# Optimization experiments

Hardware: AMD Instinct MI355X
Metric: run time of the kernel (lower is better)

## Reference

```python
import jax, jax.numpy as jnp
import numpy as np

N_LAYERS = 4
N, D = 50000, 80          # nodes, hidden (hardcoded 80 in Net)
E, ED = 800000, 16        # edges, edge_attr dim
PE_DIM = 37               # pe_embedding=37
G = 256                   # number of graphs in the batch
MSG = 2 * D + ED          # per-edge message dim: cat([x_i, x_j, edge_attr]) = 176
AGG = 4 * MSG             # mean/min/max/std -> 704
SCL = 3 * AGG             # identity/amplification/attenuation -> 2112
EPS_BN = 1e-5

# `deg` init kwarg: degree histogram; PNAConvSimple uses avg log-degree for scalers
_DEG_HIST = np.array([0, 5000, 10000, 15000, 10000, 5000, 3000, 2000], dtype=np.float64)
_ds = np.arange(len(_DEG_HIST), dtype=np.float64)
AVG_LOG_DEG = float((np.log(_ds + 1.0) * _DEG_HIST).sum() / _DEG_HIST.sum())


def setup_inputs() -> dict:
    key = jax.random.key(0)
    ks = jax.random.split(key, 20)
    sd = 0.05
    inp = {
        "x": jax.random.normal(ks[0], (N, D), jnp.float32),
        "edge_index": jax.random.randint(ks[1], (2, E), 0, N, jnp.int32),
        "edge_attr": jax.random.normal(ks[2], (E, ED), jnp.float32),
        "PE": jax.random.normal(ks[3], (N, PE_DIM), jnp.float32),
        "snorm": jnp.ones((N, 1), jnp.float32),
        "batch": jnp.sort(jax.random.randint(ks[4], (N,), 0, G, jnp.int32)),
        # per-layer params (stacked over 4 layers)
        "pe_w": jax.random.normal(ks[5], (N_LAYERS, PE_DIM, D), jnp.float32) * sd,
        "pe_b": jnp.zeros((N_LAYERS, D), jnp.float32),
        "conv_w": jax.random.normal(ks[6], (N_LAYERS, SCL, D), jnp.float32) * sd,
        "conv_b": jnp.zeros((N_LAYERS, D), jnp.float32),
        "bn_g": jnp.ones((N_LAYERS, D), jnp.float32),
        "bn_b": jnp.zeros((N_LAYERS, D), jnp.float32),
        # MLP head 80 -> 40 -> 20 -> 1
        "w1": jax.random.normal(ks[7], (D, 40), jnp.float32) * sd,
        "b1": jnp.zeros((40,), jnp.float32),
        "w2": jax.random.normal(ks[8], (40, 20), jnp.float32) * sd,
        "b2": jnp.zeros((20,), jnp.float32),
        "w3": jax.random.normal(ks[9], (20, 1), jnp.float32) * sd,
        "b3": jnp.zeros((1,), jnp.float32),
    }
    return inp


def _pna_layer(x, src, tgt, edge_attr, pe, pe_w, pe_b, W, b, g, beta):
    # node features enriched with PE embedding (pe_embedding=37 -> 80)
    xp = x + pe @ pe_w + pe_b                                  # [N, D]
    h = jnp.concatenate([xp[tgt], xp[src], edge_attr], axis=-1)  # [E, MSG]
    one = jnp.ones((h.shape[0],), h.dtype)
    cnt = jax.ops.segment_sum(one, tgt, N)
    d = jnp.maximum(cnt, 1.0)[:, None]                         # in-degree, clamped >= 1
    s = jax.ops.segment_sum(h, tgt, N)
    mean = s / d
    sq = jax.ops.segment_sum(h * h, tgt, N) / d
    std = jnp.sqrt(jax.nn.relu(sq - mean * mean) + 1e-5)
    mx = jax.ops.segment_max(h, tgt, N)
    mx = jnp.where(jnp.isfinite(mx), mx, 0.0)
    mn = jax.ops.segment_min(h, tgt, N)
    mn = jnp.where(jnp.isfinite(mn), mn, 0.0)
    agg = jnp.concatenate([mean, mn, mx, std], axis=-1)        # [N, AGG]
    logd = jnp.log(d + 1.0)
    out = jnp.concatenate(
        [agg, agg * (logd / AVG_LOG_DEG), agg * (AVG_LOG_DEG / logd)], axis=-1
    )                                                          # [N, SCL]
    out = out @ W + b                                          # post_nn Linear -> [N, D]
    # BatchNorm over nodes (batch statistics; deterministic)
    mu = out.mean(0)
    var = out.var(0)
    out = (out - mu) * jax.lax.rsqrt(var + EPS_BN) * g + beta
    return jax.nn.relu(out) + x                                # residual (dropout off in eval)


def reference(x, edge_index, edge_attr, PE, snorm, batch,
              pe_w, pe_b, conv_w, conv_b, bn_g, bn_b,
              w1, b1, w2, b2, w3, b3):
    src, tgt = edge_index[0], edge_index[1]
    for l in range(N_LAYERS):
        x = _pna_layer(x, src, tgt, edge_attr, PE,
                       pe_w[l], pe_b[l], conv_w[l], conv_b[l], bn_g[l], bn_b[l])
    # global_mean_pool over graphs
    gcnt = jnp.maximum(jax.ops.segment_sum(jnp.ones((N,), x.dtype), batch, G), 1.0)[:, None]
    pooled = jax.ops.segment_sum(x, batch, G) / gcnt           # [G, D]
    h = jax.nn.relu(pooled @ w1 + b1)
    h = jax.nn.relu(h @ w2 + b2)
    return h @ w3 + b3                                         # [G, 1]
```

## Files before the change

### kernel.cpp

```cpp
#include <hip/hip_runtime.h>
#include <stdint.h>

#define NN 50000
#define DD 80
#define NE 800000
#define EDIM 16
#define PED 37
#define NG 256
#define NLAY 4
#define KZ 480
#define NOUT 240
#define MPAD 50048
#define NBLK (MPAD/128)
#define NB 196
#define KP 64
#define NPE (NLAY*DD)
#define AVG_LD 1.4059212841460147f
#define S5 0.0031622776601683794f

typedef __bf16 bf16x8 __attribute__((ext_vector_type(8)));
typedef float f32x4 __attribute__((ext_vector_type(4)));

__device__ __forceinline__ unsigned short f2bf(float f){
  union { float f; unsigned u; } v; v.f = f;
  return (unsigned short)((v.u + 0x7fffu + ((v.u >> 16) & 1u)) >> 16);
}
__device__ __forceinline__ float bf2f(unsigned short u){
  union { unsigned u; float f; } v; v.u = ((unsigned)u) << 16; return v.f;
}
__device__ __forceinline__ unsigned packbf(float a, float b){
  return (unsigned)f2bf(a) | ((unsigned)f2bf(b) << 16);
}

#define R_HIST NE
#define R_ZP8  (((MPAD-NN)*KZ)/8)
#define R_WP   (NLAY*NOUT*KZ)
#define R_PEB  (MPAD*KP)
#define R_PWT  (NPE*KP)
#define R_TOT  (R_HIST + R_ZP8 + R_WP + R_PEB + R_PWT)

__global__ void k_init(const int* __restrict__ ei, int* deg, unsigned short* Z,
                       const float* __restrict__ conv_w, unsigned short* __restrict__ WcT,
                       const float* __restrict__ PE,
                       const float* __restrict__ pe_w, const float* __restrict__ pe_b,
                       unsigned short* __restrict__ PEb, unsigned short* __restrict__ pwT){
  int idx = blockIdx.x*blockDim.x + threadIdx.x;
  if(idx < R_HIST){ atomicAdd(&deg[ei[NE + idx]], 1); return; }
  int r1 = idx - R_HIST;
  if(r1 < R_ZP8){
    uint4* zp = (uint4*)(Z + (size_t)NN*KZ);
    zp[r1] = (uint4){0,0,0,0};
    return;
  }
  int r2 = r1 - R_ZP8;
  if(r2 < R_WP){
    int l = r2 / (NOUT*KZ);
    int k = r2 % (NOUT*KZ);
    int j = k / KZ;
    int r = k % KZ;
    int ks = j / DD, c = j % DD;
    const float* cw = conv_w + (size_t)l*2112*DD;
    float val = 0.0f;
    if(r < 384){
      int stat = r/96, m = r%96;
      val = cw[(size_t)(ks*704 + stat*176 + 80 + m)*DD + c];
    } else if(r < 464){
      int m = r - 384;
      int b = ks*704 + m;
      val = cw[(size_t)b*DD + c] + cw[(size_t)(b+176)*DD + c] + cw[(size_t)(b+352)*DD + c];
    } else if(r == 464){
      float s = 0.0f; int b = ks*704 + 528;
      for(int m=0;m<80;++m) s += cw[(size_t)(b+m)*DD + c];
      val = S5 * s;
    }
    WcT[(size_t)l*NOUT*KZ + k] = f2bf(val);
    return;
  }
  int r3 = r2 - R_WP;
  if(r3 < R_PEB){
    int i = r3 / KP, k = r3 % KP;
    float v = 0.0f;
    if(i < NN){
      if(k < PED) v = PE[(size_t)i*PED + k];
      else if(k == PED) v = 1.0f;
    }
    PEb[r3] = f2bf(v);
    return;
  }
  int r4 = r3 - R_PEB;
  if(r4 < R_PWT){
    int j = r4 / KP, k = r4 % KP;
    int l = j / DD, c = j % DD;
    float v = 0.0f;
    if(k < PED) v = pe_w[(size_t)(l*PED + k)*DD + c];
    else if(k == PED) v = pe_b[l*DD + c];
    pwT[r4] = f2bf(v);
  }
}

__global__ __launch_bounds__(256) void k_pegemm(
    const unsigned short* __restrict__ PEb, const unsigned short* __restrict__ pwT,
    const float* __restrict__ x0, unsigned short* __restrict__ pe_all,
    unsigned short* __restrict__ xpb){
  int tid = threadIdx.x;
  int wave = tid >> 6, lane = tid & 63;
  int r = lane & 15, q = lane >> 4;
  int m0 = blockIdx.x*64 + wave*16;
  const unsigned short* Ap = PEb + (size_t)(m0 + r)*KP + q*8;
  const unsigned short* Bp = pwT + (size_t)r*KP + q*8;
  f32x4 acc[20];
  #pragma unroll
  for(int i=0;i<20;++i) acc[i] = (f32x4){0.f,0.f,0.f,0.f};
  #pragma unroll
  for(int k0=0; k0<KP; k0+=32){
    bf16x8 a = *(const bf16x8*)(Ap + k0);
    #pragma unroll
    for(int ct=0; ct<20; ++ct){
      bf16x8 b = *(const bf16x8*)(Bp + (size_t)ct*16*KP + k0);
      acc[ct] = __builtin_amdgcn_mfma_f32_16x16x32_bf16(a, b, acc[ct], 0, 0, 0);
    }
  }
  #pragma unroll
  for(int rr=0; rr<4; ++rr){
    int grow = m0 + q*4 + rr;
    #pragma unroll
    for(int ct=0; ct<20; ++ct){
      int c = ct*16 + r;
      float v = acc[ct][rr];
      pe_all[(size_t)grow*NPE + c] = f2bf(v);
      if(c < DD && grow < NN)
        xpb[(size_t)grow*DD + c] = f2bf(x0[(size_t)grow*DD + c] + v);
    }
  }
}

__global__ void k_scan1(const int* __restrict__ deg, int* bsum){
  __shared__ int red[256];
  int i = blockIdx.x*256 + threadIdx.x;
  int v = (i < NN) ? deg[i] : 0;
  red[threadIdx.x] = v; __syncthreads();
  for(int d=128; d>0; d>>=1){
    if(threadIdx.x < d) red[threadIdx.x] += red[threadIdx.x + d];
    __syncthreads();
  }
  if(threadIdx.x == 0) bsum[blockIdx.x] = red[0];
}

__global__ void k_scan2(const int* __restrict__ bsum, int* bbase, int* off){
  __shared__ int s[256];
  int t = threadIdx.x;
  int v = (t < NB) ? bsum[t] : 0;
  s[t] = v; __syncthreads();
  for(int d=1; d<256; d<<=1){
    int u = (t >= d) ? s[t-d] : 0;
    __syncthreads();
    s[t] += u;
    __syncthreads();
  }
  if(t < NB) bbase[t] = s[t] - v;
  if(t == NB-1) off[NN] = s[t];
}

__global__ void k_scan3(const int* __restrict__ deg, const int* __restrict__ bbase,
                        int* off, int* pos){
  __shared__ int s[256];
  int t = threadIdx.x;
  int i = blockIdx.x*256 + t;
  int v = (i < NN) ? deg[i] : 0;
  s[t] = v; __syncthreads();
  for(int d=1; d<256; d<<=1){
    int u = (t >= d) ? s[t-d] : 0;
    __syncthreads();
    s[t] += u;
    __syncthreads();
  }
  int excl = s[t] - v + bbase[blockIdx.x];
  if(i < NN){ off[i] = excl; pos[i] = excl; }
}

__global__ void k_fill(const int* __restrict__ ei, const float* __restrict__ ea,
                       int* pos, int* esrc, unsigned short* __restrict__ ea_b){
  int e = blockIdx.x*blockDim.x + threadIdx.x;
  if(e >= NE) return;
  int t = ei[NE + e];
  int idx = atomicAdd(&pos[t], 1);
  esrc[idx] = ei[e];
  const float4* s = (const float4*)(ea + (size_t)e*EDIM);
  float4 f0=s[0], f1=s[1], f2=s[2], f3=s[3];
  unsigned short tmp[16];
  tmp[0]=f2bf(f0.x); tmp[1]=f2bf(f0.y); tmp[2]=f2bf(f0.z); tmp[3]=f2bf(f0.w);
  tmp[4]=f2bf(f1.x); tmp[5]=f2bf(f1.y); tmp[6]=f2bf(f1.z); tmp[7]=f2bf(f1.w);
  tmp[8]=f2bf(f2.x); tmp[9]=f2bf(f2.y); tmp[10]=f2bf(f2.z); tmp[11]=f2bf(f2.w);
  tmp[12]=f2bf(f3.x); tmp[13]=f2bf(f3.y); tmp[14]=f2bf(f3.z); tmp[15]=f2bf(f3.w);
  uint4* d = (uint4*)(ea_b + (size_t)idx*EDIM);
  d[0] = *(uint4*)&tmp[0];
  d[1] = *(uint4*)&tmp[8];
}

__global__ __launch_bounds__(256) void k_agg(
    const unsigned short* __restrict__ xpb, const unsigned short* __restrict__ ea_b,
    const int* __restrict__ esrc, const int* __restrict__ off,
    unsigned short* __restrict__ Z, float2* __restrict__ sc){
  int g = blockIdx.x*4 + (threadIdx.x >> 6);
  if(g >= NN) return;
  int lane = threadIdx.x & 63;
  int h = lane >> 5, t = lane & 31;
  int lo = off[g], hi = off[g+1];
  int d = hi - lo;
  float s0=0,s1=0,s2=0,q0=0,q1=0,q2=0;
  const float INF = __builtin_huge_valf();
  float mn0=INF,mn1=INF,mn2=INF,mx0=-INF,mx1=-INF,mx2=-INF;

  auto edge = [&](int j){
    int sr = esrc[j];
    const unsigned* xr32 = (const unsigned*)(xpb + (size_t)sr*DD);
    unsigned w = xr32[t];
    union {unsigned u; float f;} ua, ub;
    ua.u = w << 16; ub.u = w & 0xffff0000u;
    float v0 = ua.f, v1 = ub.f;
    unsigned short u2 = (t < 16) ? xpb[(size_t)sr*DD + 64 + t]
                                 : ea_b[(size_t)j*EDIM + (t - 16)];
    float v2 = bf2f(u2);
    s0+=v0; q0+=v0*v0; mn0=fminf(mn0,v0); mx0=fmaxf(mx0,v0);
    s1+=v1; q1+=v1*v1; mn1=fminf(mn1,v1); mx1=fmaxf(mx1,v1);
    s2+=v2; q2+=v2*v2; mn2=fminf(mn2,v2); mx2=fmaxf(mx2,v2);
  };
  int j = lo + h;
  for(; j + 2 < hi; j += 4){ edge(j); edge(j+2); }
  if(j < hi) edge(j);

  s0 += __shfl_xor(s0,32,64); s1 += __shfl_xor(s1,32,64); s2 += __shfl_xor(s2,32,64);
  q0 += __shfl_xor(q0,32,64); q1 += __shfl_xor(q1,32,64); q2 += __shfl_xor(q2,32,64);
  mn0 = fminf(mn0, __shfl_xor(mn0,32,64));
  mn1 = fminf(mn1, __shfl_xor(mn1,32,64));
  mn2 = fminf(mn2, __shfl_xor(mn2,32,64));
  mx0 = fmaxf(mx0, __shfl_xor(mx0,32,64));
  mx1 = fmaxf(mx1, __shfl_xor(mx1,32,64));
  mx2 = fmaxf(mx2, __shfl_xor(mx2,32,64));

  float dc = (float)(d>0?d:1);
  float inv = 1.0f/dc;
  float m0=s0*inv, m1=s1*inv, m2=s2*inv;
  float sd0 = sqrtf(fmaxf(q0*inv - m0*m0, 0.0f) + 1e-5f);
  float sd1 = sqrtf(fmaxf(q1*inv - m1*m1, 0.0f) + 1e-5f);
  float sd2 = sqrtf(fmaxf(q2*inv - m2*m2, 0.0f) + 1e-5f);
  if(d==0){ mn0=mn1=mn2=0.0f; mx0=mx1=mx2=0.0f; }

  unsigned* zr32 = (unsigned*)(Z + (size_t)g*KZ);
  unsigned short* zr = (unsigned short*)zr32;
  if(h == 0){
    zr32[t]       = packbf(m0, m1);
    zr32[48 + t]  = packbf(mn0, mn1);
    zr32[96 + t]  = packbf(mx0, mx1);
    zr32[144 + t] = packbf(sd0, sd1);
    zr[64 + t]        = f2bf(m2);
    zr[96 + 64 + t]   = f2bf(mn2);
    zr[192 + 64 + t]  = f2bf(mx2);
    zr[288 + 64 + t]  = f2bf(sd2);
  } else {
    const unsigned* xg32 = (const unsigned*)(xpb + (size_t)g*DD);
    zr32[192 + t] = (d>0) ? xg32[t] : 0u;
    if(t < 8)  zr32[224 + t] = (d>0) ? xg32[32 + t] : 0u;
    if(t >= 8 && t < 16) zr32[232 + (t-8)] = (t==8) ? 0x3F80u : 0u;
  }
  if(lane == 0){
    float logd = logf(dc + 1.0f);
    sc[g] = make_float2(logd/AVG_LD, AVG_LD/logd);
  }
}

__global__ __launch_bounds__(256) void k_gemm(
    const unsigned short* __restrict__ Z, const unsigned short* __restrict__ WcT,
    const float2* __restrict__ sc, const float* __restrict__ bias,
    float* __restrict__ outb, float* __restrict__ partial){
  __shared__ float sred[4][160];
  int tid = threadIdx.x;
  int wave = tid >> 6, lane = tid & 63;
  int r = lane & 15, q = lane >> 4;
  int m0 = blockIdx.x*128 + wave*32;
  const unsigned short* Ap = Z + (size_t)(m0 + r)*KZ + q*8;
  const unsigned short* Bp = WcT + (size_t)r*KZ + q*8;
  f32x4 acc0[15], acc1[15];
  #pragma unroll
  for(int i=0;i<15;++i){ acc0[i]=(f32x4){0.f,0.f,0.f,0.f}; acc1[i]=(f32x4){0.f,0.f,0.f,0.f}; }
  #pragma unroll 1
  for(int k0=0; k0<KZ; k0+=32){
    bf16x8 a0 = *(const bf16x8*)(Ap + k0);
    bf16x8 a1 = *(const bf16x8*)(Ap + 16*KZ + k0);
    #pragma unroll
    for(int ct=0; ct<15; ++ct){
      bf16x8 b = *(const bf16x8*)(Bp + (size_t)ct*16*KZ + k0);
      acc0[ct] = __builtin_amdgcn_mfma_f32_16x16x32_bf16(a0, b, acc0[ct], 0, 0, 0);
      acc1[ct] = __builtin_amdgcn_mfma_f32_16x16x32_bf16(a1, b, acc1[ct], 0, 0, 0);
    }
  }
  float colS[5], colQ[5];
  #pragma unroll
  for(int ct=0; ct<5; ++ct){ colS[ct]=0.f; colQ[ct]=0.f; }
  #pragma unroll
  for(int rr=0; rr<4; ++rr){
    int grow = m0 + q*4 + rr;
    if(grow < NN){
      float2 ab = sc[grow];
      #pragma unroll
      for(int ct=0; ct<5; ++ct){
        int c = ct*16 + r;
        float v = acc0[ct][rr] + ab.x*acc0[ct+5][rr] + ab.y*acc0[ct+10][rr] + bias[c];
        outb[(size_t)grow*DD + c] = v;
        colS[ct] += v; colQ[ct] += v*v;
      }
    }
  }
  #pragma unroll
  for(int rr=0; rr<4; ++rr){
    int grow = m0 + 16 + q*4 + rr;
    if(grow < NN){
      float2 ab = sc[grow];
      #pragma unroll
      for(int ct=0; ct<5; ++ct){
        int c = ct*16 + r;
        float v = acc1[ct][rr] + ab.x*acc1[ct+5][rr] + ab.y*acc1[ct+10][rr] + bias[c];
        outb[(size_t)grow*DD + c] = v;
        colS[ct] += v; colQ[ct] += v*v;
      }
    }
  }
  #pragma unroll
  for(int ct=0; ct<5; ++ct){
    colS[ct] += __shfl_xor(colS[ct], 16, 64);
    colS[ct] += __shfl_xor(colS[ct], 32, 64);
    colQ[ct] += __shfl_xor(colQ[ct], 16, 64);
    colQ[ct] += __shfl_xor(colQ[ct], 32, 64);
  }
  if(q == 0){
    #pragma unroll
    for(int ct=0; ct<5; ++ct){
      int c = ct*16 + r;
      sred[wave][c] = colS[ct];
      sred[wave][80+c] = colQ[ct];
    }
  }
  __syncthreads();
  if(tid < 160){
    partial[(size_t)blockIdx.x*160 + tid] =
      sred[0][tid] + sred[1][tid] + sred[2][tid] + sred[3][tid];
  }
}

__global__ void k_bnfin(const float* __restrict__ partial, float* __restrict__ murs){
  __shared__ float red[1024];
  __shared__ float tot[160];
  int tid = threadIdx.x;
  int c = tid % 160, stripe = tid / 160;
  float s = 0.0f;
  if(tid < 960){
    for(int b=stripe; b<NBLK; b+=6) s += partial[(size_t)b*160 + c];
  }
  red[tid] = s; __syncthreads();
  if(tid < 160){
    float t2 = 0.0f;
    for(int k=0;k<6;++k) t2 += red[k*160 + tid];
    tot[tid] = t2;
  }
  __syncthreads();
  if(tid < 80){
    float mu = tot[tid] / (float)NN;
    float var = tot[80+tid] / (float)NN - mu*mu;
    murs[tid] = mu;
    murs[80+tid] = rsqrtf(var + 1e-5f);
  }
}

__global__ __launch_bounds__(256) void k_apply(
    const float* __restrict__ outb, const float* __restrict__ murs,
    const float* __restrict__ g_, const float* __restrict__ b_,
    const float* __restrict__ xc, float* __restrict__ xn,
    const unsigned short* __restrict__ pe_all, unsigned short* __restrict__ xpb,
    int lnext, int do_xp){
  int idx = blockIdx.x*blockDim.x + threadIdx.x;
  if(idx >= NN*20) return;
  int c = (idx % 20) * 4;
  float4 o = ((const float4*)outb)[idx];
  float4 x = ((const float4*)xc)[idx];
  float4 r;
  r.x = fmaxf((o.x - murs[c+0])*murs[80+c+0]*g_[c+0] + b_[c+0], 0.0f) + x.x;
  r.y = fmaxf((o.y - murs[c+1])*murs[80+c+1]*g_[c+1] + b_[c+1], 0.0f) + x.y;
  r.z = fmaxf((o.z - murs[c+2])*murs[80+c+2]*g_[c+2] + b_[c+2], 0.0f) + x.z;
  r.w = fmaxf((o.w - murs[c+3])*murs[80+c+3]*g_[c+3] + b_[c+3], 0.0f) + x.w;
  ((float4*)xn)[idx] = r;
  if(do_xp){
    int i = idx / 20;
    uint2 pe = ((const uint2*)pe_all)[(size_t)i*(NPE/4) + lnext*(DD/4) + (idx % 20)];
    float p0 = bf2f((unsigned short)(pe.x & 0xffffu));
    float p1 = bf2f((unsigned short)(pe.x >> 16));
    float p2 = bf2f((unsigned short)(pe.y & 0xffffu));
    float p3 = bf2f((unsigned short)(pe.y >> 16));
    uint2 out;
    out.x = packbf(r.x + p0, r.y + p1);
    out.y = packbf(r.z + p2, r.w + p3);
    ((uint2*)xpb)[idx] = out;
  }
}

__device__ __forceinline__ int lbound(const int* b, int n, int v){
  int lo=0, hi=n;
  while(lo < hi){ int mid = (lo+hi)>>1; if(b[mid] < v) lo = mid+1; else hi = mid; }
  return lo;
}

__global__ __launch_bounds__(640) void k_poolmlp(
    const float* __restrict__ xf, const int* __restrict__ batch,
    const float* __restrict__ w1, const float* __restrict__ b1,
    const float* __restrict__ w2, const float* __restrict__ b2,
    const float* __restrict__ w3, const float* __restrict__ b3,
    float* __restrict__ out){
  __shared__ float red[8][80];
  __shared__ float pooled[80];
  __shared__ float h1[40], h2[20];
  int g = blockIdx.x;
  int tid = threadIdx.x;
  int stripe = tid / 80, c = tid % 80;
  int lo = lbound(batch, NN, g), hi = lbound(batch, NN, g+1);
  float s = 0.0f;
  for(int i = lo + stripe; i < hi; i += 8) s += xf[(size_t)i*DD + c];
  red[stripe][c] = s;
  __syncthreads();
  if(tid < 80){
    float tsum = 0.0f;
    #pragma unroll
    for(int k=0;k<8;++k) tsum += red[k][tid];
    int cnt = hi - lo;
    pooled[tid] = tsum / (float)(cnt > 0 ? cnt : 1);
  }
  __syncthreads();
  if(tid < 40){
    float h = b1[tid];
    for(int cc=0; cc<80; ++cc) h += pooled[cc] * w1[cc*40 + tid];
    h1[tid] = fmaxf(h, 0.0f);
  }
  __syncthreads();
  if(tid < 20){
    float h = b2[tid];
    for(int cc=0; cc<40; ++cc) h += h1[cc] * w2[cc*20 + tid];
    h2[tid] = fmaxf(h, 0.0f);
  }
  __syncthreads();
  if(tid == 0){
    float o = b3[0];
    for(int j=0;j<20;++j) o += h2[j] * w3[j];
    out[g] = o;
  }
}

extern "C" void kernel_launch(void* const* d_in, const int* in_sizes, int n_in,
                              void* d_out, int out_size, void* d_ws, size_t ws_size,
                              hipStream_t stream){
  const float* x0     = (const float*)d_in[0];
  const int*   ei     = (const int*)d_in[1];
  const float* ea     = (const float*)d_in[2];
  const float* PE     = (const float*)d_in[3];
  const int*   batch  = (const int*)d_in[5];
  const float* pe_w   = (const float*)d_in[6];
  const float* pe_b   = (const float*)d_in[7];
  const float* conv_w = (const float*)d_in[8];
  const float* conv_b = (const float*)d_in[9];
  const float* bn_g   = (const float*)d_in[10];
  const float* bn_b   = (const float*)d_in[11];
  const float* w1 = (const float*)d_in[12];
  const float* b1 = (const float*)d_in[13];
  const float* w2 = (const float*)d_in[14];
  const float* b2 = (const float*)d_in[15];
  const float* w3 = (const float*)d_in[16];
  const float* b3 = (const float*)d_in[17];
  float* dout = (float*)d_out;

  char* p = (char*)d_ws;
  auto alloc = [&](size_t bytes)->char*{
    char* r = p; p += (bytes + 255) & ~(size_t)255; return r;
  };
  int* deg  = (int*)alloc((size_t)NN*4);
  int* pos  = (int*)alloc((size_t)NN*4);
  int* off  = (int*)alloc((size_t)(NN+1)*4);
  int* bsum = (int*)alloc((size_t)NB*4);
  int* bbase= (int*)alloc((size_t)NB*4);
  int* esrc = (int*)alloc((size_t)NE*4);
  unsigned short* ea_b = (unsigned short*)alloc((size_t)NE*EDIM*2);
  unsigned short* xpb  = (unsigned short*)alloc((size_t)NN*DD*2);
  unsigned short* PEb  = (unsigned short*)alloc((size_t)MPAD*KP*2);
  unsigned short* pwT  = (unsigned short*)alloc((size_t)NPE*KP*2);
  unsigned short* pe_all = (unsigned short*)alloc((size_t)MPAD*NPE*2);
  unsigned short* Z    = (unsigned short*)alloc((size_t)MPAD*KZ*2);
  unsigned short* WcT  = (unsigned short*)alloc((size_t)NLAY*NOUT*KZ*2);
  float* outb = (float*)alloc((size_t)NN*DD*4);
  float* xA   = (float*)alloc((size_t)NN*DD*4);
  float* xB   = (float*)alloc((size_t)NN*DD*4);
  float2* sc  = (float2*)alloc((size_t)MPAD*8);
  float* partial = (float*)alloc((size_t)NBLK*160*4);
  float* murs = (float*)alloc(160*4);

  hipMemsetAsync(deg, 0, (size_t)NN*4, stream);
  k_init<<<(R_TOT+255)/256, 256, 0, stream>>>(ei, deg, Z, conv_w, WcT, PE, pe_w, pe_b,
                                              PEb, pwT);
  k_pegemm<<<MPAD/64, 256, 0, stream>>>(PEb, pwT, x0, pe_all, xpb);
  k_scan1<<<NB, 256, 0, stream>>>(deg, bsum);
  k_scan2<<<1, 256, 0, stream>>>(bsum, bbase, off);
  k_scan3<<<NB, 256, 0, stream>>>(deg, bbase, off, pos);
  k_fill<<<(NE+255)/256, 256, 0, stream>>>(ei, ea, pos, esrc, ea_b);

  const float* xc = x0;
  float* bufs[2] = {xA, xB};
  for(int l=0; l<NLAY; ++l){
    float* xn = bufs[l & 1];
    k_agg<<<(NN+3)/4, 256, 0, stream>>>(xpb, ea_b, esrc, off, Z, sc);
    k_gemm<<<NBLK, 256, 0, stream>>>(Z, WcT + (size_t)l*NOUT*KZ, sc, conv_b + l*DD,
                                     outb, partial);
    k_bnfin<<<1, 1024, 0, stream>>>(partial, murs);
    int do_xp = (l < NLAY-1) ? 1 : 0;
    int lnext = (l+1 < NLAY) ? l+1 : 0;
    k_apply<<<(NN*20+255)/256, 256, 0, stream>>>(outb, murs, bn_g + l*DD, bn_b + l*DD,
                                                 xc, xn, pe_all, xpb, lnext, do_xp);
    xc = xn;
  }
  k_poolmlp<<<NG, 640, 0, stream>>>(xc, batch, w1, b1, w2, b2, w3, b3, dout);
}
```

Baseline: 638.8 us.

## Pack edge source index with edge attrs; fold BN finalize into GEMM atomics

Edge source indices and bf16 edge attributes are interleaved into a single 64-byte per-edge record, so the aggregation kernel reads one record per edge instead of two separate arrays. The BN statistics reduction is also changed: GEMM blocks atomically add their column sums into a per-layer stats buffer, and each apply block computes mean and rstd itself, which removes the single-block k_bnfin launch per layer. The cost is more per-edge traffic from the padded records, float atomics that make the stats order-dependent, and redundant mean/rstd computation in every apply block.

```diff
diff --git a/kernel.cpp b/kernel.cpp
--- a/kernel.cpp
+++ b/kernel.cpp
@@ -15,6 +15,7 @@
 #define NB 196
 #define KP 64
 #define NPE (NLAY*DD)
+#define EREC 32
 #define AVG_LD 1.4059212841460147f
 #define S5 0.0031622776601683794f
 
@@ -179,28 +180,33 @@
 }
 
 __global__ void k_fill(const int* __restrict__ ei, const float* __restrict__ ea,
-                       int* pos, int* esrc, unsigned short* __restrict__ ea_b){
+                       int* pos, unsigned short* __restrict__ erec){
   int e = blockIdx.x*blockDim.x + threadIdx.x;
   if(e >= NE) return;
   int t = ei[NE + e];
   int idx = atomicAdd(&pos[t], 1);
-  esrc[idx] = ei[e];
   const float4* s = (const float4*)(ea + (size_t)e*EDIM);
   float4 f0=s[0], f1=s[1], f2=s[2], f3=s[3];
-  unsigned short tmp[16];
+  unsigned short tmp[32];
   tmp[0]=f2bf(f0.x); tmp[1]=f2bf(f0.y); tmp[2]=f2bf(f0.z); tmp[3]=f2bf(f0.w);
   tmp[4]=f2bf(f1.x); tmp[5]=f2bf(f1.y); tmp[6]=f2bf(f1.z); tmp[7]=f2bf(f1.w);
   tmp[8]=f2bf(f2.x); tmp[9]=f2bf(f2.y); tmp[10]=f2bf(f2.z); tmp[11]=f2bf(f2.w);
   tmp[12]=f2bf(f3.x); tmp[13]=f2bf(f3.y); tmp[14]=f2bf(f3.z); tmp[15]=f2bf(f3.w);
-  uint4* d = (uint4*)(ea_b + (size_t)idx*EDIM);
+  *(int*)&tmp[16] = ei[e];
+  *(int*)&tmp[18] = 0;
+  *(uint4*)&tmp[20] = (uint4){0,0,0,0};
+  *(uint4*)&tmp[28] = (uint4){0,0,0,0};
+  uint4* d = (uint4*)(erec + (size_t)idx*EREC);
   d[0] = *(uint4*)&tmp[0];
   d[1] = *(uint4*)&tmp[8];
+  d[2] = *(uint4*)&tmp[16];
+  d[3] = *(uint4*)&tmp[24];
 }
 
 __global__ __launch_bounds__(256) void k_agg(
-    const unsigned short* __restrict__ xpb, const unsigned short* __restrict__ ea_b,
-    const int* __restrict__ esrc, const int* __restrict__ off,
-    unsigned short* __restrict__ Z, float2* __restrict__ sc){
+    const unsigned short* __restrict__ xpb, const unsigned short* __restrict__ erec,
+    const int* __restrict__ off, unsigned short* __restrict__ Z,
+    float2* __restrict__ sc){
   int g = blockIdx.x*4 + (threadIdx.x >> 6);
   if(g >= NN) return;
   int lane = threadIdx.x & 63;
@@ -212,14 +218,14 @@
   float mn0=INF,mn1=INF,mn2=INF,mx0=-INF,mx1=-INF,mx2=-INF;
 
   auto edge = [&](int j){
-    int sr = esrc[j];
+    const unsigned short* er = erec + (size_t)j*EREC;
+    int sr = *(const int*)(er + 16);
     const unsigned* xr32 = (const unsigned*)(xpb + (size_t)sr*DD);
     unsigned w = xr32[t];
     union {unsigned u; float f;} ua, ub;
     ua.u = w << 16; ub.u = w & 0xffff0000u;
     float v0 = ua.f, v1 = ub.f;
-    unsigned short u2 = (t < 16) ? xpb[(size_t)sr*DD + 64 + t]
-                                 : ea_b[(size_t)j*EDIM + (t - 16)];
+    unsigned short u2 = (t < 16) ? xpb[(size_t)sr*DD + 64 + t] : er[t - 16];
     float v2 = bf2f(u2);
     s0+=v0; q0+=v0*v0; mn0=fminf(mn0,v0); mx0=fmaxf(mx0,v0);
     s1+=v1; q1+=v1*v1; mn1=fminf(mn1,v1); mx1=fmaxf(mx1,v1);
@@ -272,7 +278,7 @@
 __global__ __launch_bounds__(256) void k_gemm(
     const unsigned short* __restrict__ Z, const unsigned short* __restrict__ WcT,
     const float2* __restrict__ sc, const float* __restrict__ bias,
-    float* __restrict__ outb, float* __restrict__ partial){
+    float* __restrict__ outb, float* __restrict__ stats){
   __shared__ float sred[4][160];
   int tid = threadIdx.x;
   int wave = tid >> 6, lane = tid & 63;
@@ -342,42 +348,26 @@
   }
   __syncthreads();
   if(tid < 160){
-    partial[(size_t)blockIdx.x*160 + tid] =
-      sred[0][tid] + sred[1][tid] + sred[2][tid] + sred[3][tid];
-  }
-}
-
-__global__ void k_bnfin(const float* __restrict__ partial, float* __restrict__ murs){
-  __shared__ float red[1024];
-  __shared__ float tot[160];
-  int tid = threadIdx.x;
-  int c = tid % 160, stripe = tid / 160;
-  float s = 0.0f;
-  if(tid < 960){
-    for(int b=stripe; b<NBLK; b+=6) s += partial[(size_t)b*160 + c];
-  }
-  red[tid] = s; __syncthreads();
-  if(tid < 160){
-    float t2 = 0.0f;
-    for(int k=0;k<6;++k) t2 += red[k*160 + tid];
-    tot[tid] = t2;
-  }
-  __syncthreads();
-  if(tid < 80){
-    float mu = tot[tid] / (float)NN;
-    float var = tot[80+tid] / (float)NN - mu*mu;
-    murs[tid] = mu;
-    murs[80+tid] = rsqrtf(var + 1e-5f);
+    atomicAdd(&stats[tid], sred[0][tid] + sred[1][tid] + sred[2][tid] + sred[3][tid]);
   }
 }
 
 __global__ __launch_bounds__(256) void k_apply(
-    const float* __restrict__ outb, const float* __restrict__ murs,
+    const float* __restrict__ outb, const float* __restrict__ stats,
     const float* __restrict__ g_, const float* __restrict__ b_,
     const float* __restrict__ xc, float* __restrict__ xn,
     const unsigned short* __restrict__ pe_all, unsigned short* __restrict__ xpb,
     int lnext, int do_xp){
-  int idx = blockIdx.x*blockDim.x + threadIdx.x;
+  __shared__ float murs[160];
+  int tid = threadIdx.x;
+  if(tid < 80){
+    float mu = stats[tid] / (float)NN;
+    float var = stats[80+tid] / (float)NN - mu*mu;
+    murs[tid] = mu;
+    murs[80+tid] = rsqrtf(var + 1e-5f);
+  }
+  __syncthreads();
+  int idx = blockIdx.x*blockDim.x + tid;
   if(idx >= NN*20) return;
   int c = (idx % 20) * 4;
   float4 o = ((const float4*)outb)[idx];
@@ -483,8 +473,8 @@
   int* off  = (int*)alloc((size_t)(NN+1)*4);
   int* bsum = (int*)alloc((size_t)NB*4);
   int* bbase= (int*)alloc((size_t)NB*4);
-  int* esrc = (int*)alloc((size_t)NE*4);
-  unsigned short* ea_b = (unsigned short*)alloc((size_t)NE*EDIM*2);
+  float* stats4 = (float*)alloc((size_t)NLAY*160*4);
+  unsigned short* erec = (unsigned short*)alloc((size_t)NE*EREC*2);
   unsigned short* xpb  = (unsigned short*)alloc((size_t)NN*DD*2);
   unsigned short* PEb  = (unsigned short*)alloc((size_t)MPAD*KP*2);
   unsigned short* pwT  = (unsigned short*)alloc((size_t)NPE*KP*2);
@@ -495,29 +485,28 @@
   float* xA   = (float*)alloc((size_t)NN*DD*4);
   float* xB   = (float*)alloc((size_t)NN*DD*4);
   float2* sc  = (float2*)alloc((size_t)MPAD*8);
-  float* partial = (float*)alloc((size_t)NBLK*160*4);
-  float* murs = (float*)alloc(160*4);
 
   hipMemsetAsync(deg, 0, (size_t)NN*4, stream);
+  hipMemsetAsync(stats4, 0, (size_t)NLAY*160*4, stream);
   k_init<<<(R_TOT+255)/256, 256, 0, stream>>>(ei, deg, Z, conv_w, WcT, PE, pe_w, pe_b,
                                               PEb, pwT);
   k_pegemm<<<MPAD/64, 256, 0, stream>>>(PEb, pwT, x0, pe_all, xpb);
   k_scan1<<<NB, 256, 0, stream>>>(deg, bsum);
   k_scan2<<<1, 256, 0, stream>>>(bsum, bbase, off);
   k_scan3<<<NB, 256, 0, stream>>>(deg, bbase, off, pos);
-  k_fill<<<(NE+255)/256, 256, 0, stream>>>(ei, ea, pos, esrc, ea_b);
+  k_fill<<<(NE+255)/256, 256, 0, stream>>>(ei, ea, pos, erec);
 
   const float* xc = x0;
   float* bufs[2] = {xA, xB};
   for(int l=0; l<NLAY; ++l){
     float* xn = bufs[l & 1];
-    k_agg<<<(NN+3)/4, 256, 0, stream>>>(xpb, ea_b, esrc, off, Z, sc);
+    float* stats = stats4 + l*160;
+    k_agg<<<(NN+3)/4, 256, 0, stream>>>(xpb, erec, off, Z, sc);
     k_gemm<<<NBLK, 256, 0, stream>>>(Z, WcT + (size_t)l*NOUT*KZ, sc, conv_b + l*DD,
-                                     outb, partial);
-    k_bnfin<<<1, 1024, 0, stream>>>(partial, murs);
+                                     outb, stats);
     int do_xp = (l < NLAY-1) ? 1 : 0;
     int lnext = (l+1 < NLAY) ? l+1 : 0;
-    k_apply<<<(NN*20+255)/256, 256, 0, stream>>>(outb, murs, bn_g + l*DD, bn_b + l*DD,
+    k_apply<<<(NN*20+255)/256, 256, 0, stream>>>(outb, stats, bn_g + l*DD, bn_b + l*DD,
                                                  xc, xn, pe_all, xpb, lnext, do_xp);
     xc = xn;
   }
```

New measurement: 590.3 us. 7.6% less time.
